# Optimization experiments

Hardware: AMD Instinct MI355X
Metric: run time of the kernel (lower is better)

## Reference

```python
import jax, jax.numpy as jnp
import numpy as np

B, T = 128, 512          # batch, sequence length (padded game length)
F_IN = 19 * 19           # flattened Go board features
H = 128                  # n_hid
P = 19 * 19 + 1          # policy classes: board points + pass


def setup_inputs() -> dict:
    key = jax.random.key(0)
    ks = jax.random.split(key, 8)
    s = 0.05  # init scale
    return {
        "states": jax.random.normal(ks[0], (B, T, F_IN), jnp.float32),
        "moves": jax.random.randint(ks[1], (B, T), 0, P, jnp.int32),
        "values": jax.random.uniform(ks[2], (B, T), jnp.float32, -1.0, 1.0),
        # LSTM layer 0: concat([x, h]) @ W0 + b0, gates [i, f, g, o]
        "W0": jax.random.normal(ks[3], (F_IN + H, 4 * H), jnp.float32) * s,
        "b0": jnp.zeros((4 * H,), jnp.float32),
        # LSTM layer 1
        "W1": jax.random.normal(ks[4], (H + H, 4 * H), jnp.float32) * s,
        "b1": jnp.zeros((4 * H,), jnp.float32),
        # policy head (size**2 + 1 logits), value head (tanh scalar)
        "Wp": jax.random.normal(ks[5], (H, P), jnp.float32) * s,
        "bp": jnp.zeros((P,), jnp.float32),
        "Wv": jax.random.normal(ks[6], (H, 1), jnp.float32) * s,
        "bv": jnp.zeros((1,), jnp.float32),
    }


def _lstm_cell(h, c, x, W, b):
    # TF LSTMCell: z = [x; h] @ W + b, forget bias 1.0
    z = jnp.concatenate([x, h], axis=-1) @ W + b
    i, f, g, o = jnp.split(z, 4, axis=-1)
    c_new = jax.nn.sigmoid(f + 1.0) * c + jax.nn.sigmoid(i) * jnp.tanh(g)
    h_new = jax.nn.sigmoid(o) * jnp.tanh(c_new)
    return h_new, c_new


def reference(states, moves, values, W0, b0, W1, b1, Wp, bp, Wv, bv):
    b = states.shape[0]
    zeros = jnp.zeros((b, H), states.dtype)

    def step(carry, x_t):
        h0, c0, h1, c1 = carry
        h0, c0 = _lstm_cell(h0, c0, x_t, W0, b0)
        h1, c1 = _lstm_cell(h1, c1, h0, W1, b1)
        return (h0, c0, h1, c1), h1

    _, hs = jax.lax.scan(step, (zeros, zeros, zeros, zeros),
                         jnp.swapaxes(states, 0, 1))  # hs: [T, B, H]
    outputs = jnp.swapaxes(hs, 0, 1)                  # [B, T, H]

    policy_logits = outputs @ Wp + bp                 # [B, T, P]
    winners = jnp.tanh(outputs @ Wv + bv)[..., 0]     # [B, T]

    mask = (values != -9.0).astype(jnp.float32)
    n_mask = mask.sum()

    logp = jax.nn.log_softmax(policy_logits, axis=-1)
    xent = -jnp.take_along_axis(logp, moves[..., None].astype(jnp.int32), axis=-1)[..., 0]
    policy_loss = (mask * xent).sum() / n_mask
    value_loss = (mask * jnp.square(winners - values)).sum() / n_mask
    acc = (moves == jnp.argmax(policy_logits, axis=-1).astype(moves.dtype)).astype(jnp.float32).mean()
    return jnp.stack([policy_loss, value_loss, acc])
```

## Files before the change

### kernel.cpp

```cpp
#include <hip/hip_runtime.h>
#include <hip/hip_bf16.h>
#include <stdint.h>


typedef short v8s __attribute__((ext_vector_type(8)));
typedef float v4f __attribute__((ext_vector_type(4)));
typedef int   v8i __attribute__((ext_vector_type(8)));
typedef float f4u __attribute__((ext_vector_type(4), aligned(4)));

#define MFMA_B16(a,b,c) __builtin_amdgcn_mfma_f32_16x16x32_bf16((a),(b),(c),0,0,0)
#define MFMA_MX(a,b,c) \
  __builtin_amdgcn_mfma_scale_f32_16x16x128_f8f6f4((a),(b),(c),0,0,0,0x7F7F7F7F,0,0x7F7F7F7F)

#define NT     512
#define FIN    361
#define KP0    384
#define NPC    362
#define NPP    368

#define OFF_Z    ((size_t)0)
#define OFF_H1   ((size_t)83886080)
#define OFF_W0XT ((size_t)100663296)
#define OFF_WPT  ((size_t)101187584)
#define OFF_B0P  ((size_t)101281792)
#define OFF_BPP  ((size_t)101285888)
#define OFF_ACC  ((size_t)101287936)

static __device__ __forceinline__ short f2b(float f) {
  __hip_bfloat16 h = __float2bfloat16(f);
  union { __hip_bfloat16 h; short s; } cv; cv.h = h; return cv.s;
}
static __device__ __forceinline__ float b2f(unsigned int lo16) {
  union { unsigned u; float f; } cv; cv.u = lo16 << 16; return cv.f;
}
static __device__ __forceinline__ unsigned f2e4m3(float f) {
  union { float f; unsigned u; } cv; cv.f = f;
  unsigned s = (cv.u >> 31) << 7;
  float a = fabsf(f);
  a = fminf(a, 448.f);
  unsigned code;
  if (a >= 0.015625f) {
    union { float f; unsigned u; } m; m.f = a;
    unsigned u = m.u + 0x7FFFF + ((m.u >> 20) & 1);
    code = (u >> 20) - 960;
    if (code > 126u) code = 126u;
  } else {
    code = (unsigned)rintf(a * 512.f);
  }
  return s | code;
}
static __device__ __forceinline__ unsigned f2e4m3_fast(float f) {
#if __has_builtin(__builtin_amdgcn_cvt_pk_fp8_f32)
  return (unsigned)__builtin_amdgcn_cvt_pk_fp8_f32(f, f, 0, false) & 0xffu;
#else
  return f2e4m3(f);
#endif
}

static __device__ __forceinline__ void sync_lds() {
  __builtin_amdgcn_sched_barrier(0);
  asm volatile("s_waitcnt lgkmcnt(0)" ::: "memory");
  __builtin_amdgcn_s_barrier();
  __builtin_amdgcn_sched_barrier(0);
}

__global__ __launch_bounds__(256) void k_conv_weights(
    const float* __restrict__ W0, const float* __restrict__ b0,
    const float* __restrict__ Wp, const float* __restrict__ bp,
    char* __restrict__ ws) {
  int idx = blockIdx.x * 256 + threadIdx.x;
  __hip_bfloat16* W0xT = (__hip_bfloat16*)(ws + OFF_W0XT);
  __hip_bfloat16* WpT  = (__hip_bfloat16*)(ws + OFF_WPT);
  float* b0p = (float*)(ws + OFF_B0P);
  float* bpp = (float*)(ws + OFF_BPP);
  float* acc = (float*)(ws + OFF_ACC);

  if (idx < 196608) {
    int np = idx / 384, k = idx - np * 384;
    int n = (np >> 2) + 128 * (np & 3);
    float v = (k < FIN) ? W0[(size_t)k * 512 + n] : 0.f;
    W0xT[idx] = __float2bfloat16(v);
    return;
  }
  idx -= 196608;
  if (idx < 47104) {
    int p = idx >> 7, k = idx & 127;
    WpT[idx] = __float2bfloat16(p < NPC ? Wp[(size_t)k * NPC + p] : 0.f);
    return;
  }
  idx -= 47104;
  if (idx < 512) {
    int n = (idx >> 2) + 128 * (idx & 3);
    b0p[idx] = b0[n] + (((idx & 3) == 1) ? 1.0f : 0.0f);
    return;
  }
  idx -= 512;
  if (idx < NPP) { bpp[idx] = (idx < NPC) ? bp[idx] : -1e30f; return; }
  idx -= NPP;
  if (idx < 4) { acc[idx] = 0.f; return; }
}

template<int KTOT, bool AF32>
__global__ __launch_bounds__(256) void k_gemm(
    const void* __restrict__ Ap, const __hip_bfloat16* __restrict__ BT,
    const float* __restrict__ bias, __hip_bfloat16* __restrict__ C) {
  __shared__ char sm[65536];
  const int tid = threadIdx.x;
  const int l = tid & 63, wm = tid >> 6;
  const int c = l & 15, lg = l >> 4;
  const int m0 = blockIdx.x * 128;
  const int n0 = blockIdx.y * 128;
  constexpr int NS = KTOT / 64;

  uint4 ra[4], rb[4];
  float fa[32];

  auto LD = [&](int ks) {
#pragma unroll
    for (int i = 0; i < 4; i++) {
      int idx = i * 4096 + tid * 16;
      int row = idx >> 7, colb = idx & 127;
      if constexpr (AF32) {
        int r = m0 + row;
        const float* src = (const float*)Ap + ((size_t)(r & 127) * NT + (r >> 7)) * FIN;
        int kb = ks * 64 + (colb >> 1);
        if (kb + 8 <= FIN) {
          f4u a0 = *(const f4u*)(src + kb);
          f4u a1 = *(const f4u*)(src + kb + 4);
#pragma unroll
          for (int u = 0; u < 4; u++) { fa[i * 8 + u] = a0[u]; fa[i * 8 + 4 + u] = a1[u]; }
        } else {
#pragma unroll
          for (int u = 0; u < 8; u++) {
            int kf = kb + u;
            fa[i * 8 + u] = (kf < FIN) ? src[kf] : 0.f;
          }
        }
      } else {
        ra[i] = *(const uint4*)((const char*)Ap + ((size_t)(m0 + row) * KTOT + ks * 64) * 2 + colb);
      }
      rb[i] = *(const uint4*)((const char*)BT + ((size_t)(n0 + row) * KTOT + ks * 64) * 2 + colb);
    }
  };
  auto ST = [&](int bsel) {
#pragma unroll
    for (int i = 0; i < 4; i++) {
      int idx = i * 4096 + tid * 16;
      int row = idx >> 7, colb = idx & 127;
      int sw = colb ^ ((row & 7) << 4);
      if constexpr (AF32) {
        v8s w;
#pragma unroll
        for (int u = 0; u < 8; u++) w[u] = f2b(fa[i * 8 + u]);
        *(v8s*)(sm + bsel * 16384 + row * 128 + sw) = w;
      } else {
        *(uint4*)(sm + bsel * 16384 + row * 128 + sw) = ra[i];
      }
      *(uint4*)(sm + 32768 + bsel * 16384 + row * 128 + sw) = rb[i];
    }
  };

  v4f acc[2][8];
  v4f z4 = {0.f, 0.f, 0.f, 0.f};
#pragma unroll
  for (int mt = 0; mt < 2; mt++)
#pragma unroll
    for (int nt = 0; nt < 8; nt++) acc[mt][nt] = z4;

  LD(0); ST(0);
  __syncthreads();
  for (int ks = 0; ks < NS; ks++) {
    if (ks + 1 < NS) LD(ks + 1);
    const int bsel = ks & 1;
#pragma unroll
    for (int kk = 0; kk < 2; kk++) {
      int bir = kk * 64 + lg * 16;
      v8s af[2];
#pragma unroll
      for (int mt = 0; mt < 2; mt++) {
        int row = wm * 32 + mt * 16 + c;
        af[mt] = *(v8s*)(sm + bsel * 16384 + row * 128 + (bir ^ ((row & 7) << 4)));
      }
#pragma unroll
      for (int nt = 0; nt < 8; nt++) {
        int n = nt * 16 + c;
        v8s bf = *(v8s*)(sm + 32768 + bsel * 16384 + n * 128 + (bir ^ ((n & 7) << 4)));
#pragma unroll
        for (int mt = 0; mt < 2; mt++) acc[mt][nt] = MFMA_B16(af[mt], bf, acc[mt][nt]);
      }
    }
    if (ks + 1 < NS) ST((ks + 1) & 1);
    __syncthreads();
  }

#pragma unroll
  for (int mt = 0; mt < 2; mt++)
#pragma unroll
    for (int nt = 0; nt < 8; nt++) {
      int colp = n0 + nt * 16 + c;
      float bs = bias[colp];
#pragma unroll
      for (int j = 0; j < 4; j++) {
        int row = m0 + wm * 32 + mt * 16 + lg * 4 + j;
        C[(size_t)row * 512 + colp] = __float2bfloat16(acc[mt][nt][j] + bs);
      }
    }
}

__global__ __launch_bounds__(1024, 4) void k_scan12(
    const __hip_bfloat16* __restrict__ Z, const float* __restrict__ W0f,
    const float* __restrict__ W1f, const float* __restrict__ b1,
    __hip_bfloat16* __restrict__ h1out) {
  __shared__ char sm[8192];
  const int tid = threadIdx.x;
  const int l = tid & 63, wv = tid >> 6;
  const int c = l & 15, lg = l >> 4;
  const int role = wv >> 3, rw = wv & 7;
  const int B0 = blockIdx.x * 4;
  const int m_ = 16 * rw + c;
  const int row = 4 * lg;
  const int wf8 = row * 128 + (((m_ >> 3) ^ row) << 3) + (m_ & 7);

  for (int e = tid * 4; e < 8192; e += 1024 * 4) *(int*)(sm + e) = 0;

  auto AFRAG = [&](int base) -> v8i {
    union { unsigned long long q[4]; v8i v; } u;
#pragma unroll
    for (int t = 0; t < 4; t++)
      u.q[t] = *(const unsigned long long*)(
          sm + base + c * 128 + ((((lg * 4 + t) ^ c) & 15) << 3));
    return u.v;
  };

  if (role == 0) {
    v8i breg[4];
#pragma unroll
    for (int g = 0; g < 4; g++) {
      int n = g * 128 + m_;
      union { unsigned long long q[4]; v8i v; } u;
#pragma unroll
      for (int t = 0; t < 4; t++) {
        unsigned long long w = 0ull;
#pragma unroll
        for (int j = 0; j < 8; j++) {
          int k = lg * 32 + t * 8 + j;
          w |= (unsigned long long)f2e4m3(W0f[(size_t)(FIN + k) * 512 + n]) << (8 * j);
        }
        u.q[t] = w;
      }
      breg[g] = u.v;
    }

    uint2 zA, zB, zC;
    auto ZLD = [&](int t) -> uint2 {
      return *(const uint2*)(Z + ((size_t)t * 128 + B0 + lg) * 512 + m_ * 4);
    };
    zA = ZLD(0); zB = ZLD(1);
    float cst = 0.f;
    __syncthreads();

    for (int s = 0; s < NT; s++) {
      v8i av = AFRAG(((s + 1) & 1) * 2048);
      v4f acc[4];
#pragma unroll
      for (int g = 0; g < 4; g++) acc[g] = (v4f){0.f, 0.f, 0.f, 0.f};
#pragma unroll
      for (int g = 0; g < 4; g++) acc[g] = MFMA_MX(av, breg[g], acc[g]);
      if (s + 2 < NT) zC = ZLD(s + 2);

      float xi = acc[0][0] + b2f(zA.x & 0xffffu);
      float xf = acc[1][0] + b2f(zA.x >> 16);
      float xg = acc[2][0] + b2f(zA.y & 0xffffu);
      float xo = acc[3][0] + b2f(zA.y >> 16);
      float ei = __expf(-xi);
      float ef = __expf(-xf);
      float eg = __expf(2.f * xg);
      float eo = __expf(-xo);
      float cn = cst * __builtin_amdgcn_rcpf(1.f + ef)
               + (eg - 1.f) * __builtin_amdgcn_rcpf((1.f + ei) * (eg + 1.f));
      cst = cn;
      float ec = __expf(2.f * cn);
      float hv = (ec - 1.f) * __builtin_amdgcn_rcpf((1.f + eo) * (ec + 1.f));
      *(unsigned char*)(sm + (s & 1) * 2048 + wf8) = (unsigned char)f2e4m3_fast(hv);
      zA = zB; zB = zC;
      sync_lds();
    }
    sync_lds();
  } else {
    v8i bregH[4], bregX[4];
#pragma unroll
    for (int g = 0; g < 4; g++) {
      int n = g * 128 + m_;
      union { unsigned long long q[4]; v8i v; } uh, ux;
#pragma unroll
      for (int t = 0; t < 4; t++) {
        unsigned long long wh = 0ull, wx = 0ull;
#pragma unroll
        for (int j = 0; j < 8; j++) {
          int k = lg * 32 + t * 8 + j;
          wh |= (unsigned long long)f2e4m3(W1f[(size_t)(128 + k) * 512 + n]) << (8 * j);
          wx |= (unsigned long long)f2e4m3(W1f[(size_t)k * 512 + n]) << (8 * j);
        }
        uh.q[t] = wh; ux.q[t] = wx;
      }
      bregH[g] = uh.v; bregX[g] = ux.v;
    }
    float bq[4];
#pragma unroll
    for (int g = 0; g < 4; g++)
      bq[g] = b1[g * 128 + m_] + ((g == 1) ? 1.0f : 0.0f);
    float cst = 0.f;
    __syncthreads();
    sync_lds();

    for (int s = 1; s <= NT; s++) {
      v8i ah = AFRAG(4096 + (s & 1) * 2048);
      v8i ax = AFRAG(((s + 1) & 1) * 2048);
      v4f acc[4];
#pragma unroll
      for (int g = 0; g < 4; g++) acc[g] = (v4f){bq[g], bq[g], bq[g], bq[g]};
#pragma unroll
      for (int g = 0; g < 4; g++) acc[g] = MFMA_MX(ah, bregH[g], acc[g]);
#pragma unroll
      for (int g = 0; g < 4; g++) acc[g] = MFMA_MX(ax, bregX[g], acc[g]);

      float xi = acc[0][0], xf = acc[1][0], xg = acc[2][0], xo = acc[3][0];
      float ei = __expf(-xi);
      float ef = __expf(-xf);
      float eg = __expf(2.f * xg);
      float eo = __expf(-xo);
      float cn = cst * __builtin_amdgcn_rcpf(1.f + ef)
               + (eg - 1.f) * __builtin_amdgcn_rcpf((1.f + ei) * (eg + 1.f));
      cst = cn;
      float ec = __expf(2.f * cn);
      float hv = (ec - 1.f) * __builtin_amdgcn_rcpf((1.f + eo) * (ec + 1.f));
      *(unsigned char*)(sm + 4096 + ((s + 1) & 1) * 2048 + wf8) =
          (unsigned char)f2e4m3_fast(hv);
      union { short s; __hip_bfloat16 h; } cv; cv.s = f2b(hv);
      h1out[((size_t)(s - 1) * 128 + B0 + lg) * 128 + m_] = cv.h;
      sync_lds();
    }
  }
}

__global__ __launch_bounds__(256) void k_heads(
    const __hip_bfloat16* __restrict__ Hh, const __hip_bfloat16* __restrict__ WpT,
    const float* __restrict__ bpp, const float* __restrict__ Wv,
    const float* __restrict__ bv, const int* __restrict__ moves,
    const float* __restrict__ values, float* __restrict__ accum) {
  __shared__ char sm[110592];
  const int tid = threadIdx.x;
  const int l = tid & 63, wm = tid >> 6;
  const int c = l & 15, lg = l >> 4;
  const int r0 = blockIdx.x * 64;

#pragma unroll
  for (int i = 0; i < 4; i++) {
    int idx = i * 4096 + tid * 16;
    int row = idx >> 8, colb = idx & 255;
    uint4 v = *(const uint4*)((const char*)Hh + (size_t)r0 * 256 + idx);
    *(uint4*)(sm + row * 256 + (colb ^ ((row & 7) << 4))) = v;
  }
#pragma unroll
  for (int i = 0; i < 23; i++) {
    int idx = i * 4096 + tid * 16;
    int row = idx >> 8, colb = idx & 255;
    uint4 v = *(const uint4*)((const char*)WpT + idx);
    *(uint4*)(sm + 16384 + row * 256 + (colb ^ ((row & 7) << 4))) = v;
  }
  __syncthreads();

  v4f acc[23];
  v4f z4 = {0.f, 0.f, 0.f, 0.f};
#pragma unroll
  for (int q = 0; q < 23; q++) acc[q] = z4;
#pragma unroll
  for (int kk = 0; kk < 4; kk++) {
    int bir = kk * 64 + lg * 16;
    int ar = wm * 16 + c;
    v8s a = *(v8s*)(sm + ar * 256 + (bir ^ ((ar & 7) << 4)));
#pragma unroll
    for (int q = 0; q < 23; q++) {
      int n = q * 16 + c;
      v8s b = *(v8s*)(sm + 16384 + n * 256 + (bir ^ ((n & 7) << 4)));
      acc[q] = MFMA_B16(a, b, acc[q]);
    }
  }
  float bq[23];
#pragma unroll
  for (int q = 0; q < 23; q++) bq[q] = bpp[q * 16 + c];

  float tp = 0.f, tv = 0.f, ta = 0.f, tn = 0.f;
#pragma unroll
  for (int j = 0; j < 4; j++) {
    int rloc = lg * 4 + j;
    int r = r0 + wm * 16 + rloc;
    int t = r >> 7, b = r & 127;
    int mv = moves[(size_t)b * NT + t];
    float val = values[(size_t)b * NT + t];
    float msk = (val != -9.0f) ? 1.f : 0.f;

    float pmax = -3.0e38f;
#pragma unroll
    for (int q = 0; q < 23; q++) pmax = fmaxf(pmax, acc[q][j] + bq[q]);
#pragma unroll
    for (int d = 1; d < 16; d <<= 1) pmax = fmaxf(pmax, __shfl_xor(pmax, d, 64));
    float ps = 0.f;
#pragma unroll
    for (int q = 0; q < 23; q++) ps += __expf((acc[q][j] + bq[q]) - pmax);
#pragma unroll
    for (int d = 1; d < 16; d <<= 1) ps += __shfl_xor(ps, d, 64);
    float lse = pmax + __logf(ps);

    int qm = mv >> 4, cm = mv & 15;
    float mlv = 0.f;
#pragma unroll
    for (int q = 0; q < 23; q++) if (q == qm) mlv = acc[q][j] + bq[q];
    mlv = __shfl(mlv, (l & 48) + cm, 64);
    float xent = lse - mlv;

    float amx = -3.0e38f; int aix = 0;
#pragma unroll
    for (int q = 0; q < 23; q++) {
      float v = acc[q][j] + bq[q];
      if (v > amx) { amx = v; aix = q * 16 + c; }
    }
#pragma unroll
    for (int d = 1; d < 16; d <<= 1) {
      float ov = __shfl_xor(amx, d, 64);
      int oi = __shfl_xor(aix, d, 64);
      if (ov > amx || (ov == amx && oi < aix)) { amx = ov; aix = oi; }
    }

    float pd = 0.f;
    int vrow = wm * 16 + rloc;
#pragma unroll
    for (int i = 0; i < 8; i++) {
      int k = c * 8 + i;
      short hv = *(short*)(sm + vrow * 256 + ((k * 2) ^ ((vrow & 7) << 4)));
      pd += b2f((unsigned short)hv) * Wv[k];
    }
#pragma unroll
    for (int d = 1; d < 16; d <<= 1) pd += __shfl_xor(pd, d, 64);
    float eo = __expf(2.f * (pd + bv[0]));
    float win = (eo - 1.f) * __builtin_amdgcn_rcpf(eo + 1.f);
    float dv = win - val;

    if (c == 0) {
      tp += msk * xent;
      tv += msk * dv * dv;
      ta += (aix == mv) ? 1.f : 0.f;
      tn += msk;
    }
  }
  tp += __shfl_xor(tp, 16, 64); tp += __shfl_xor(tp, 32, 64);
  tv += __shfl_xor(tv, 16, 64); tv += __shfl_xor(tv, 32, 64);
  ta += __shfl_xor(ta, 16, 64); ta += __shfl_xor(ta, 32, 64);
  tn += __shfl_xor(tn, 16, 64); tn += __shfl_xor(tn, 32, 64);
  if (l == 0) {
    atomicAdd(accum + 0, tp);
    atomicAdd(accum + 1, tv);
    atomicAdd(accum + 2, ta);
    atomicAdd(accum + 3, tn);
  }
}

__global__ void k_final(const float* __restrict__ accum, float* __restrict__ out) {
  if (threadIdx.x == 0) {
    float nm = accum[3];
    out[0] = accum[0] / nm;
    out[1] = accum[1] / nm;
    out[2] = accum[2] / 65536.0f;
  }
}

extern "C" void kernel_launch(void* const* d_in, const int* in_sizes, int n_in,
                              void* d_out, int out_size, void* d_ws, size_t ws_size,
                              hipStream_t stream) {
  (void)in_sizes; (void)n_in; (void)out_size; (void)ws_size;
  const float* states = (const float*)d_in[0];
  const int*   moves  = (const int*)d_in[1];
  const float* values = (const float*)d_in[2];
  const float* W0 = (const float*)d_in[3];
  const float* b0 = (const float*)d_in[4];
  const float* W1 = (const float*)d_in[5];
  const float* b1 = (const float*)d_in[6];
  const float* Wp = (const float*)d_in[7];
  const float* bp = (const float*)d_in[8];
  const float* Wv = (const float*)d_in[9];
  const float* bv = (const float*)d_in[10];
  char* ws = (char*)d_ws;

  __hip_bfloat16* zbuf = (__hip_bfloat16*)(ws + OFF_Z);
  __hip_bfloat16* h1   = (__hip_bfloat16*)(ws + OFF_H1);
  __hip_bfloat16* W0xT = (__hip_bfloat16*)(ws + OFF_W0XT);
  __hip_bfloat16* WpT  = (__hip_bfloat16*)(ws + OFF_WPT);
  float* b0p = (float*)(ws + OFF_B0P);
  float* bpp = (float*)(ws + OFF_BPP);
  float* acc = (float*)(ws + OFF_ACC);

  k_conv_weights<<<956, 256, 0, stream>>>(W0, b0, Wp, bp, ws);
  k_gemm<KP0, true><<<dim3(512, 4), 256, 0, stream>>>(states, W0xT, b0p, zbuf);
  k_scan12<<<32, 1024, 0, stream>>>(zbuf, W0, W1, b1, h1);
  k_heads<<<1024, 256, 0, stream>>>(h1, WpT, bpp, Wv, bv, moves, values, acc);
  k_final<<<1, 1, 0, stream>>>(acc, (float*)d_out);
}
```

Before: 824.5 us.

## Load and convert states once per block; fold final reduction into heads kernel

The input projection GEMM now gives each block one timestep's full 128x384 A tile. That tile is converted from fp32 to bf16 once and kept in LDS while the block loops over all four N tiles. Before, the fp32 states were read and converted four times, once per N-tile block. The separate finalization kernel is removed: the last heads block, found with an atomic ticket counter, computes the outputs. In exchange the GEMM uses 128KB of LDS with fewer, larger blocks, which lowers occupancy.

```diff
diff --git a/kernel.cpp b/kernel.cpp
--- a/kernel.cpp
+++ b/kernel.cpp
@@ -17,6 +17,7 @@
 #define KP0    384
 #define NPC    362
 #define NPP    368
+#define AG __HIP_MEMORY_SCOPE_AGENT
 
 #define OFF_Z    ((size_t)0)
 #define OFF_H1   ((size_t)83886080)
@@ -97,114 +98,103 @@
   idx -= 512;
   if (idx < NPP) { bpp[idx] = (idx < NPC) ? bp[idx] : -1e30f; return; }
   idx -= NPP;
-  if (idx < 4) { acc[idx] = 0.f; return; }
-}
-
-template<int KTOT, bool AF32>
-__global__ __launch_bounds__(256) void k_gemm(
-    const void* __restrict__ Ap, const __hip_bfloat16* __restrict__ BT,
+  if (idx < 8) { acc[idx] = 0.f; return; }
+}
+
+__global__ __launch_bounds__(512) void k_gemm2(
+    const float* __restrict__ states, const __hip_bfloat16* __restrict__ BT,
     const float* __restrict__ bias, __hip_bfloat16* __restrict__ C) {
-  __shared__ char sm[65536];
+  __shared__ char sm[131072];
   const int tid = threadIdx.x;
-  const int l = tid & 63, wm = tid >> 6;
+  const int l = tid & 63, wv = tid >> 6;
   const int c = l & 15, lg = l >> 4;
-  const int m0 = blockIdx.x * 128;
-  const int n0 = blockIdx.y * 128;
-  constexpr int NS = KTOT / 64;
-
-  uint4 ra[4], rb[4];
-  float fa[32];
-
-  auto LD = [&](int ks) {
-#pragma unroll
-    for (int i = 0; i < 4; i++) {
-      int idx = i * 4096 + tid * 16;
+  const int t_ = blockIdx.x;
+
+  auto SWA = [](int row, int byo) {
+    return (byo & ~127) + ((byo & 127) ^ ((((byo >> 7) ^ row) & 7) << 4));
+  };
+
+  {
+    const int arow = tid >> 2, q = tid & 3;
+    const float* src = states + ((size_t)arow * NT + t_) * FIN;
+#pragma unroll
+    for (int j = 0; j < 12; j++) {
+      int kb = q * 96 + j * 8;
+      v8s w;
+      if (kb + 8 <= FIN) {
+        f4u a0 = *(const f4u*)(src + kb);
+        f4u a1 = *(const f4u*)(src + kb + 4);
+#pragma unroll
+        for (int u = 0; u < 4; u++) { w[u] = f2b(a0[u]); w[4 + u] = f2b(a1[u]); }
+      } else {
+#pragma unroll
+        for (int u = 0; u < 8; u++) {
+          int kf = kb + u;
+          w[u] = f2b((kf < FIN) ? src[kf] : 0.f);
+        }
+      }
+      *(v8s*)(sm + arow * 768 + SWA(arow, kb * 2)) = w;
+    }
+  }
+
+  uint4 rb[2];
+  auto LD_B = [&](int by, int ks) {
+#pragma unroll
+    for (int i = 0; i < 2; i++) {
+      int idx = i * 8192 + tid * 16;
       int row = idx >> 7, colb = idx & 127;
-      if constexpr (AF32) {
-        int r = m0 + row;
-        const float* src = (const float*)Ap + ((size_t)(r & 127) * NT + (r >> 7)) * FIN;
-        int kb = ks * 64 + (colb >> 1);
-        if (kb + 8 <= FIN) {
-          f4u a0 = *(const f4u*)(src + kb);
-          f4u a1 = *(const f4u*)(src + kb + 4);
-#pragma unroll
-          for (int u = 0; u < 4; u++) { fa[i * 8 + u] = a0[u]; fa[i * 8 + 4 + u] = a1[u]; }
-        } else {
-#pragma unroll
-          for (int u = 0; u < 8; u++) {
-            int kf = kb + u;
-            fa[i * 8 + u] = (kf < FIN) ? src[kf] : 0.f;
-          }
+      rb[i] = *(const uint4*)((const char*)BT +
+          ((size_t)(by * 128 + row) * KP0 + ks * 64) * 2 + colb);
+    }
+  };
+  auto ST_B = [&](int bsel) {
+#pragma unroll
+    for (int i = 0; i < 2; i++) {
+      int idx = i * 8192 + tid * 16;
+      int row = idx >> 7, colb = idx & 127;
+      *(uint4*)(sm + 98304 + bsel * 16384 + row * 128 + (colb ^ ((row & 7) << 4))) = rb[i];
+    }
+  };
+
+  LD_B(0, 0); ST_B(0);
+  __syncthreads();
+
+  int st = 0;
+  for (int by = 0; by < 4; by++) {
+    v4f acc[8];
+#pragma unroll
+    for (int nt = 0; nt < 8; nt++) acc[nt] = (v4f){0.f, 0.f, 0.f, 0.f};
+    for (int ks = 0; ks < 6; ks++, st++) {
+      int byn = by, ksn = ks + 1;
+      if (ksn == 6) { ksn = 0; byn = by + 1; }
+      if (st + 1 < 24) LD_B(byn, ksn);
+      const int bsel = st & 1;
+#pragma unroll
+      for (int kk = 0; kk < 2; kk++) {
+        const int row = wv * 16 + c;
+        v8s af = *(v8s*)(sm + row * 768 + SWA(row, ks * 128 + kk * 64 + lg * 16));
+        const int bir = kk * 64 + lg * 16;
+#pragma unroll
+        for (int nt = 0; nt < 8; nt++) {
+          int n = nt * 16 + c;
+          v8s bf = *(v8s*)(sm + 98304 + bsel * 16384 + n * 128 + (bir ^ ((n & 7) << 4)));
+          acc[nt] = MFMA_B16(af, bf, acc[nt]);
         }
-      } else {
-        ra[i] = *(const uint4*)((const char*)Ap + ((size_t)(m0 + row) * KTOT + ks * 64) * 2 + colb);
       }
-      rb[i] = *(const uint4*)((const char*)BT + ((size_t)(n0 + row) * KTOT + ks * 64) * 2 + colb);
-    }
-  };
-  auto ST = [&](int bsel) {
-#pragma unroll
-    for (int i = 0; i < 4; i++) {
-      int idx = i * 4096 + tid * 16;
-      int row = idx >> 7, colb = idx & 127;
-      int sw = colb ^ ((row & 7) << 4);
-      if constexpr (AF32) {
-        v8s w;
-#pragma unroll
-        for (int u = 0; u < 8; u++) w[u] = f2b(fa[i * 8 + u]);
-        *(v8s*)(sm + bsel * 16384 + row * 128 + sw) = w;
-      } else {
-        *(uint4*)(sm + bsel * 16384 + row * 128 + sw) = ra[i];
+      if (st + 1 < 24) ST_B((st + 1) & 1);
+      __syncthreads();
+    }
+#pragma unroll
+    for (int nt = 0; nt < 8; nt++) {
+      int colp = by * 128 + nt * 16 + c;
+      float bs = bias[colp];
+#pragma unroll
+      for (int j = 0; j < 4; j++) {
+        int row = t_ * 128 + wv * 16 + lg * 4 + j;
+        C[(size_t)row * 512 + colp] = __float2bfloat16(acc[nt][j] + bs);
       }
-      *(uint4*)(sm + 32768 + bsel * 16384 + row * 128 + sw) = rb[i];
-    }
-  };
-
-  v4f acc[2][8];
-  v4f z4 = {0.f, 0.f, 0.f, 0.f};
-#pragma unroll
-  for (int mt = 0; mt < 2; mt++)
-#pragma unroll
-    for (int nt = 0; nt < 8; nt++) acc[mt][nt] = z4;
-
-  LD(0); ST(0);
-  __syncthreads();
-  for (int ks = 0; ks < NS; ks++) {
-    if (ks + 1 < NS) LD(ks + 1);
-    const int bsel = ks & 1;
-#pragma unroll
-    for (int kk = 0; kk < 2; kk++) {
-      int bir = kk * 64 + lg * 16;
-      v8s af[2];
-#pragma unroll
-      for (int mt = 0; mt < 2; mt++) {
-        int row = wm * 32 + mt * 16 + c;
-        af[mt] = *(v8s*)(sm + bsel * 16384 + row * 128 + (bir ^ ((row & 7) << 4)));
-      }
-#pragma unroll
-      for (int nt = 0; nt < 8; nt++) {
-        int n = nt * 16 + c;
-        v8s bf = *(v8s*)(sm + 32768 + bsel * 16384 + n * 128 + (bir ^ ((n & 7) << 4)));
-#pragma unroll
-        for (int mt = 0; mt < 2; mt++) acc[mt][nt] = MFMA_B16(af[mt], bf, acc[mt][nt]);
-      }
-    }
-    if (ks + 1 < NS) ST((ks + 1) & 1);
-    __syncthreads();
-  }
-
-#pragma unroll
-  for (int mt = 0; mt < 2; mt++)
-#pragma unroll
-    for (int nt = 0; nt < 8; nt++) {
-      int colp = n0 + nt * 16 + c;
-      float bs = bias[colp];
-#pragma unroll
-      for (int j = 0; j < 4; j++) {
-        int row = m0 + wm * 32 + mt * 16 + lg * 4 + j;
-        C[(size_t)row * 512 + colp] = __float2bfloat16(acc[mt][nt][j] + bs);
-      }
-    }
+    }
+  }
 }
 
 __global__ __launch_bounds__(1024, 4) void k_scan12(
@@ -347,7 +337,8 @@
     const __hip_bfloat16* __restrict__ Hh, const __hip_bfloat16* __restrict__ WpT,
     const float* __restrict__ bpp, const float* __restrict__ Wv,
     const float* __restrict__ bv, const int* __restrict__ moves,
-    const float* __restrict__ values, float* __restrict__ accum) {
+    const float* __restrict__ values, float* __restrict__ accum,
+    float* __restrict__ out) {
   __shared__ char sm[110592];
   const int tid = threadIdx.x;
   const int l = tid & 63, wm = tid >> 6;
@@ -463,14 +454,19 @@
     atomicAdd(accum + 2, ta);
     atomicAdd(accum + 3, tn);
   }
-}
-
-__global__ void k_final(const float* __restrict__ accum, float* __restrict__ out) {
-  if (threadIdx.x == 0) {
-    float nm = accum[3];
-    out[0] = accum[0] / nm;
-    out[1] = accum[1] / nm;
-    out[2] = accum[2] / 65536.0f;
+  __syncthreads();
+  if (tid == 0) {
+    int old = __hip_atomic_fetch_add((int*)(accum + 4), 1,
+                                     __ATOMIC_ACQ_REL, AG);
+    if (old == 1023) {
+      float a0 = __hip_atomic_load(accum + 0, __ATOMIC_RELAXED, AG);
+      float a1 = __hip_atomic_load(accum + 1, __ATOMIC_RELAXED, AG);
+      float a2 = __hip_atomic_load(accum + 2, __ATOMIC_RELAXED, AG);
+      float a3 = __hip_atomic_load(accum + 3, __ATOMIC_RELAXED, AG);
+      out[0] = a0 / a3;
+      out[1] = a1 / a3;
+      out[2] = a2 / 65536.0f;
+    }
   }
 }
 
@@ -500,8 +496,8 @@
   float* acc = (float*)(ws + OFF_ACC);
 
   k_conv_weights<<<956, 256, 0, stream>>>(W0, b0, Wp, bp, ws);
-  k_gemm<KP0, true><<<dim3(512, 4), 256, 0, stream>>>(states, W0xT, b0p, zbuf);
+  k_gemm2<<<512, 512, 0, stream>>>(states, W0xT, b0p, zbuf);
   k_scan12<<<32, 1024, 0, stream>>>(zbuf, W0, W1, b1, h1);
-  k_heads<<<1024, 256, 0, stream>>>(h1, WpT, bpp, Wv, bv, moves, values, acc);
-  k_final<<<1, 1, 0, stream>>>(acc, (float*)d_out);
-}
+  k_heads<<<1024, 256, 0, stream>>>(h1, WpT, bpp, Wv, bv, moves, values, acc,
+                                    (float*)d_out);
+}
```

After: 829.5 us. Within noise of the previous version (+0.6%).
